# Kernel optimization log

Measured on AMD Instinct MI355X. Metric: run time of the kernel, lower is better.

## Reference

```python
import jax, jax.numpy as jnp
import numpy as np

# Dimensions (must match init_kwargs)
IC = 8    # independent channels (one Linear each)
RC = 8    # regular channels
PC = 8    # parallel channels
G = 4     # shared-weight groups
IPG = 512 // G   # input length per group = 128
OPG = 512 // G   # output length per group = 128
B = 128


def setup_inputs() -> dict:
    key = jax.random.key(0)
    k1, k2, k3 = jax.random.split(key, 3)
    x = jax.random.normal(k1, (B, IC * RC, PC, IPG * G), dtype=jnp.float32)
    # Per-independent-channel Linear weights/biases (torch Linear: y = x @ W.T + b)
    bound = 1.0 / np.sqrt(IPG)
    W = jax.random.uniform(k2, (IC, OPG, IPG), dtype=jnp.float32, minval=-bound, maxval=bound)
    b = jax.random.uniform(k3, (IC, OPG), dtype=jnp.float32, minval=-bound, maxval=bound)
    return {"x": x, "W": W, "b": b}


def reference(x, W, b):
    Bx = x.shape[0]
    # view -> (B, IC, RC, PC, IPG*G); tensor_split along last + stack(dim=-2)
    # is a contiguous reshape -> (B, IC, RC, PC, G, IPG)
    xi = x.reshape(Bx, IC, RC, PC, G, IPG)
    # block-diagonal grouped GEMM: one Linear per independent channel i
    y = jnp.einsum('bicpgk,iok->bicpgo', xi, W) + b[None, :, None, None, None, :]
    # (B, IC, RC, PC, G, OPG) -> (B, IC*RC, PC, G*OPG)
    return y.reshape(Bx, IC * RC, PC, G * OPG)
```

## Files before the change

kernel.cpp:

```cpp
#include <hip/hip_runtime.h>
#include <hip/hip_bf16.h>

typedef __bf16 bf16x8 __attribute__((ext_vector_type(8)));
typedef __bf16 bf16x4 __attribute__((ext_vector_type(4)));
typedef float floatx4 __attribute__((ext_vector_type(4)));

#define IC 8
#define RC 8
#define PC 8
#define G_ 4
#define IPG 128
#define OPG 128

#define WROW 136
#define XROW 136

__global__ __launch_bounds__(256, 3)
void mcsl_kernel(const float* __restrict__ x,
                 const float* __restrict__ W,
                 const float* __restrict__ bias,
                 float* __restrict__ y)
{
    __shared__ __align__(16) __bf16 Wlds[128 * WROW];
    __shared__ __align__(16) __bf16 Xlds[64 * XROW];
    __shared__ float blds[128];

    const int tid = threadIdx.x;
    const int i = blockIdx.x & 7;
    const int b = blockIdx.x >> 3;

    const float* xbase = x + ((size_t)(b * (IC * RC) + i * RC)) * (PC * G_ * IPG);
    float*       ybase = y + ((size_t)(b * (IC * RC) + i * RC)) * (PC * G_ * OPG);

    const float4* Wsrc = (const float4*)(W + (size_t)i * (OPG * IPG));
    #pragma unroll
    for (int it = 0; it < 16; ++it) {
        int idx = tid + it * 256;
        float4 w4 = Wsrc[idx];
        int o  = idx >> 5;
        int k4 = (idx & 31) << 2;
        bf16x4 wq;
        wq[0] = (__bf16)w4.x; wq[1] = (__bf16)w4.y;
        wq[2] = (__bf16)w4.z; wq[3] = (__bf16)w4.w;
        *(bf16x4*)&Wlds[o * WROW + k4] = wq;
    }
    if (tid < 128) blds[tid] = bias[i * OPG + tid];

    float4 pf[8];
    {
        const float4* src = (const float4*)xbase;
        #pragma unroll
        for (int j = 0; j < 8; ++j) pf[j] = src[tid * 8 + j];
    }
    {
        const int row = tid >> 2, col0 = (tid & 3) * 32;
        #pragma unroll
        for (int j = 0; j < 4; ++j) {
            float4 a0 = pf[2 * j], a1 = pf[2 * j + 1];
            bf16x8 v;
            v[0] = (__bf16)a0.x; v[1] = (__bf16)a0.y; v[2] = (__bf16)a0.z; v[3] = (__bf16)a0.w;
            v[4] = (__bf16)a1.x; v[5] = (__bf16)a1.y; v[6] = (__bf16)a1.z; v[7] = (__bf16)a1.w;
            *(bf16x8*)&Xlds[row * XROW + col0 + j * 8] = v;
        }
    }
    __syncthreads();

    const int lane = tid & 63;
    const int wv   = tid >> 6;
    const int nrow = lane & 15;
    const int quad = lane >> 4;

    #pragma unroll
    for (int c = 0; c < 4; ++c) {
        if (c < 3) {
            const float4* src = (const float4*)(xbase + (size_t)(c + 1) * 64 * IPG);
            #pragma unroll
            for (int j = 0; j < 8; ++j) pf[j] = src[tid * 8 + j];
        }

        bf16x8 af[4];
        #pragma unroll
        for (int ks = 0; ks < 4; ++ks)
            af[ks] = *(const bf16x8*)&Xlds[(wv * 16 + nrow) * XROW + ks * 32 + quad * 8];

        floatx4 acc[8];
        #pragma unroll
        for (int ct = 0; ct < 8; ++ct) acc[ct] = (floatx4){0.f, 0.f, 0.f, 0.f};

        #pragma unroll
        for (int ks = 0; ks < 4; ++ks) {
            #pragma unroll
            for (int ct = 0; ct < 8; ++ct) {
                bf16x8 bfrag = *(const bf16x8*)&Wlds[(ct * 16 + nrow) * WROW + ks * 32 + quad * 8];
                acc[ct] = __builtin_amdgcn_mfma_f32_16x16x32_bf16(af[ks], bfrag, acc[ct], 0, 0, 0);
            }
        }

        if (c < 3) {
            __syncthreads();
            const int row = tid >> 2, col0 = (tid & 3) * 32;
            #pragma unroll
            for (int j = 0; j < 4; ++j) {
                float4 a0 = pf[2 * j], a1 = pf[2 * j + 1];
                bf16x8 v;
                v[0] = (__bf16)a0.x; v[1] = (__bf16)a0.y; v[2] = (__bf16)a0.z; v[3] = (__bf16)a0.w;
                v[4] = (__bf16)a1.x; v[5] = (__bf16)a1.y; v[6] = (__bf16)a1.z; v[7] = (__bf16)a1.w;
                *(bf16x8*)&Xlds[row * XROW + col0 + j * 8] = v;
            }
            __syncthreads();
        }

        float* yc = ybase + (size_t)c * 64 * OPG;
        const int rowl = wv * 16 + quad * 4;
        #pragma unroll
        for (int ct = 0; ct < 8; ++ct) {
            float bo = blds[ct * 16 + nrow];
            #pragma unroll
            for (int r = 0; r < 4; ++r)
                yc[(size_t)(rowl + r) * OPG + ct * 16 + nrow] = acc[ct][r] + bo;
        }
    }
}

extern "C" void kernel_launch(void* const* d_in, const int* in_sizes, int n_in,
                              void* d_out, int out_size, void* d_ws, size_t ws_size,
                              hipStream_t stream) {
    const float* x = (const float*)d_in[0];
    const float* W = (const float*)d_in[1];
    const float* b = (const float*)d_in[2];
    float* y = (float*)d_out;
    dim3 grid(1024), block(256);
    hipLaunchKernelGGL(mcsl_kernel, grid, block, 0, stream, x, W, b, y);
}
```

Measured before the change: 247.0 us.

## Hold W fragments in registers and stream X directly from global per wave

Each block now covers two batches. Every wave loads its W fragments from LDS into registers once, then streams 16-row X tiles straight from global memory into MFMA B operands. It double-buffers those loads with register prefetch, which drops the X staging through LDS and its block-wide barriers. Bias is folded into the accumulator init and the output goes out as vector nontemporal stores after swapping MFMA operand roles. In exchange the kernel uses many more registers (launch bounds cut to 2 blocks), half as many blocks, and uncoalesced-ish 32-byte global reads.

```diff
diff --git a/kernel.cpp b/kernel.cpp
--- a/kernel.cpp
+++ b/kernel.cpp
@@ -13,24 +13,19 @@
 #define OPG 128
 
 #define WROW 136
-#define XROW 136
 
-__global__ __launch_bounds__(256, 3)
+__global__ __launch_bounds__(256, 2)
 void mcsl_kernel(const float* __restrict__ x,
                  const float* __restrict__ W,
                  const float* __restrict__ bias,
                  float* __restrict__ y)
 {
     __shared__ __align__(16) __bf16 Wlds[128 * WROW];
-    __shared__ __align__(16) __bf16 Xlds[64 * XROW];
-    __shared__ float blds[128];
+    __shared__ __align__(16) float blds[128];
 
     const int tid = threadIdx.x;
     const int i = blockIdx.x & 7;
-    const int b = blockIdx.x >> 3;
-
-    const float* xbase = x + ((size_t)(b * (IC * RC) + i * RC)) * (PC * G_ * IPG);
-    float*       ybase = y + ((size_t)(b * (IC * RC) + i * RC)) * (PC * G_ * OPG);
+    const int j = blockIdx.x >> 3;
 
     const float4* Wsrc = (const float4*)(W + (size_t)i * (OPG * IPG));
     #pragma unroll
@@ -45,24 +40,6 @@
         *(bf16x4*)&Wlds[o * WROW + k4] = wq;
     }
     if (tid < 128) blds[tid] = bias[i * OPG + tid];
-
-    float4 pf[8];
-    {
-        const float4* src = (const float4*)xbase;
-        #pragma unroll
-        for (int j = 0; j < 8; ++j) pf[j] = src[tid * 8 + j];
-    }
-    {
-        const int row = tid >> 2, col0 = (tid & 3) * 32;
-        #pragma unroll
-        for (int j = 0; j < 4; ++j) {
-            float4 a0 = pf[2 * j], a1 = pf[2 * j + 1];
-            bf16x8 v;
-            v[0] = (__bf16)a0.x; v[1] = (__bf16)a0.y; v[2] = (__bf16)a0.z; v[3] = (__bf16)a0.w;
-            v[4] = (__bf16)a1.x; v[5] = (__bf16)a1.y; v[6] = (__bf16)a1.z; v[7] = (__bf16)a1.w;
-            *(bf16x8*)&Xlds[row * XROW + col0 + j * 8] = v;
-        }
-    }
     __syncthreads();
 
     const int lane = tid & 63;
@@ -70,56 +47,78 @@
     const int nrow = lane & 15;
     const int quad = lane >> 4;
 
+    bf16x8 wfrag[8][4];
     #pragma unroll
-    for (int c = 0; c < 4; ++c) {
-        if (c < 3) {
-            const float4* src = (const float4*)(xbase + (size_t)(c + 1) * 64 * IPG);
-            #pragma unroll
-            for (int j = 0; j < 8; ++j) pf[j] = src[tid * 8 + j];
-        }
-
-        bf16x8 af[4];
+    for (int ct = 0; ct < 8; ++ct)
         #pragma unroll
         for (int ks = 0; ks < 4; ++ks)
-            af[ks] = *(const bf16x8*)&Xlds[(wv * 16 + nrow) * XROW + ks * 32 + quad * 8];
+            wfrag[ct][ks] = *(const bf16x8*)&Wlds[(ct * 16 + nrow) * WROW + ks * 32 + quad * 8];
 
-        floatx4 acc[8];
-        #pragma unroll
-        for (int ct = 0; ct < 8; ++ct) acc[ct] = (floatx4){0.f, 0.f, 0.f, 0.f};
+    const int b = 2 * j + (wv >> 1);
+    const size_t slab = ((size_t)(b * (IC * RC) + i * RC)) * (PC * G_ * IPG);
+    const int rhalf = (wv & 1) * 128;
 
+    const float4* xs = (const float4*)(x + slab);
+    float*        ys = y + slab;
+
+#define TILE_SRC(T) (xs + (size_t)(rhalf + (T) * 16 + nrow) * 32 + quad * 2)
+
+    float4 pfA[8], pfB[8];
+    {
+        const float4* s0 = TILE_SRC(0);
+        const float4* s1 = TILE_SRC(1);
         #pragma unroll
         for (int ks = 0; ks < 4; ++ks) {
-            #pragma unroll
-            for (int ct = 0; ct < 8; ++ct) {
-                bf16x8 bfrag = *(const bf16x8*)&Wlds[(ct * 16 + nrow) * WROW + ks * 32 + quad * 8];
-                acc[ct] = __builtin_amdgcn_mfma_f32_16x16x32_bf16(af[ks], bfrag, acc[ct], 0, 0, 0);
-            }
+            pfA[2 * ks]     = s0[ks * 8];
+            pfA[2 * ks + 1] = s0[ks * 8 + 1];
         }
-
-        if (c < 3) {
-            __syncthreads();
-            const int row = tid >> 2, col0 = (tid & 3) * 32;
-            #pragma unroll
-            for (int j = 0; j < 4; ++j) {
-                float4 a0 = pf[2 * j], a1 = pf[2 * j + 1];
-                bf16x8 v;
-                v[0] = (__bf16)a0.x; v[1] = (__bf16)a0.y; v[2] = (__bf16)a0.z; v[3] = (__bf16)a0.w;
-                v[4] = (__bf16)a1.x; v[5] = (__bf16)a1.y; v[6] = (__bf16)a1.z; v[7] = (__bf16)a1.w;
-                *(bf16x8*)&Xlds[row * XROW + col0 + j * 8] = v;
-            }
-            __syncthreads();
-        }
-
-        float* yc = ybase + (size_t)c * 64 * OPG;
-        const int rowl = wv * 16 + quad * 4;
         #pragma unroll
-        for (int ct = 0; ct < 8; ++ct) {
-            float bo = blds[ct * 16 + nrow];
-            #pragma unroll
-            for (int r = 0; r < 4; ++r)
-                yc[(size_t)(rowl + r) * OPG + ct * 16 + nrow] = acc[ct][r] + bo;
+        for (int ks = 0; ks < 4; ++ks) {
+            pfB[2 * ks]     = s1[ks * 8];
+            pfB[2 * ks + 1] = s1[ks * 8 + 1];
         }
     }
+
+#define TILE_STEP(T, BUF, PREF) do {                                            \
+        floatx4 acc[8];                                                         \
+        _Pragma("unroll")                                                       \
+        for (int ct = 0; ct < 8; ++ct)                                          \
+            acc[ct] = *(const floatx4*)&blds[ct * 16 + quad * 4];               \
+        const float4* nsrc = (PREF) ? TILE_SRC((T) + 2) : xs;                   \
+        _Pragma("unroll")                                                       \
+        for (int ks = 0; ks < 4; ++ks) {                                        \
+            float4 a0 = BUF[2 * ks], a1 = BUF[2 * ks + 1];                      \
+            if (PREF) {                                                         \
+                BUF[2 * ks]     = nsrc[ks * 8];                                 \
+                BUF[2 * ks + 1] = nsrc[ks * 8 + 1];                             \
+            }                                                                   \
+            bf16x8 v;                                                           \
+            v[0] = (__bf16)a0.x; v[1] = (__bf16)a0.y;                           \
+            v[2] = (__bf16)a0.z; v[3] = (__bf16)a0.w;                           \
+            v[4] = (__bf16)a1.x; v[5] = (__bf16)a1.y;                           \
+            v[6] = (__bf16)a1.z; v[7] = (__bf16)a1.w;                           \
+            _Pragma("unroll")                                                   \
+            for (int ct = 0; ct < 8; ++ct)                                      \
+                acc[ct] = __builtin_amdgcn_mfma_f32_16x16x32_bf16(              \
+                              wfrag[ct][ks], v, acc[ct], 0, 0, 0);              \
+        }                                                                       \
+        float* yrow = ys + (size_t)(rhalf + (T) * 16 + nrow) * OPG + quad * 4;  \
+        _Pragma("unroll")                                                       \
+        for (int ct = 0; ct < 8; ++ct)                                          \
+            __builtin_nontemporal_store(acc[ct], (floatx4*)(yrow + ct * 16));   \
+    } while (0)
+
+    TILE_STEP(0, pfA, 1);
+    TILE_STEP(1, pfB, 1);
+    TILE_STEP(2, pfA, 1);
+    TILE_STEP(3, pfB, 1);
+    TILE_STEP(4, pfA, 1);
+    TILE_STEP(5, pfB, 1);
+    TILE_STEP(6, pfA, 0);
+    TILE_STEP(7, pfB, 0);
+
+#undef TILE_STEP
+#undef TILE_SRC
 }
 
 extern "C" void kernel_launch(void* const* d_in, const int* in_sizes, int n_in,
@@ -129,6 +128,6 @@
     const float* W = (const float*)d_in[1];
     const float* b = (const float*)d_in[2];
     float* y = (float*)d_out;
-    dim3 grid(1024), block(256);
+    dim3 grid(512), block(256);
     hipLaunchKernelGGL(mcsl_kernel, grid, block, 0, stream, x, W, b, y);
 }
```

New measurement: 249.2 us. No clear change (+0.9%).

## Load X fragments directly to registers and swap MFMA operands for vector stores

Applied to the files above, without the earlier changes.

Drops the X staging buffer in LDS. Each wave now loads its input rows straight into registers in MFMA fragment layout and converts them to bf16 there. The MFMA operands are swapped (W as A, X as B) so each lane holds four consecutive output columns, which allows 16-byte vectorized stores in place of scalar strided ones. Bias is preloaded into the accumulators, and the block-to-row mapping is changed. Less LDS per block permits a higher occupancy hint, at the risk of less coalesced global reads of x, since each lane reads 32-byte chunks spread over rows.

```diff
diff --git a/kernel.cpp b/kernel.cpp
--- a/kernel.cpp
+++ b/kernel.cpp
@@ -5,120 +5,107 @@
 typedef __bf16 bf16x4 __attribute__((ext_vector_type(4)));
 typedef float floatx4 __attribute__((ext_vector_type(4)));
 
-#define IC 8
-#define RC 8
-#define PC 8
-#define G_ 4
-#define IPG 128
-#define OPG 128
+#define WPITCH 272
 
-#define WROW 136
-#define XROW 136
-
-__global__ __launch_bounds__(256, 3)
+__global__ __launch_bounds__(256, 4)
 void mcsl_kernel(const float* __restrict__ x,
                  const float* __restrict__ W,
                  const float* __restrict__ bias,
                  float* __restrict__ y)
 {
-    __shared__ __align__(16) __bf16 Wlds[128 * WROW];
-    __shared__ __align__(16) __bf16 Xlds[64 * XROW];
-    __shared__ float blds[128];
+    __shared__ __align__(16) unsigned char Wl[128 * WPITCH];
+    __shared__ __align__(16) float blds[128];
 
-    const int tid = threadIdx.x;
-    const int i = blockIdx.x & 7;
-    const int b = blockIdx.x >> 3;
-
-    const float* xbase = x + ((size_t)(b * (IC * RC) + i * RC)) * (PC * G_ * IPG);
-    float*       ybase = y + ((size_t)(b * (IC * RC) + i * RC)) * (PC * G_ * OPG);
-
-    const float4* Wsrc = (const float4*)(W + (size_t)i * (OPG * IPG));
-    #pragma unroll
-    for (int it = 0; it < 16; ++it) {
-        int idx = tid + it * 256;
-        float4 w4 = Wsrc[idx];
-        int o  = idx >> 5;
-        int k4 = (idx & 31) << 2;
-        bf16x4 wq;
-        wq[0] = (__bf16)w4.x; wq[1] = (__bf16)w4.y;
-        wq[2] = (__bf16)w4.z; wq[3] = (__bf16)w4.w;
-        *(bf16x4*)&Wlds[o * WROW + k4] = wq;
-    }
-    if (tid < 128) blds[tid] = bias[i * OPG + tid];
-
-    float4 pf[8];
-    {
-        const float4* src = (const float4*)xbase;
-        #pragma unroll
-        for (int j = 0; j < 8; ++j) pf[j] = src[tid * 8 + j];
-    }
-    {
-        const int row = tid >> 2, col0 = (tid & 3) * 32;
-        #pragma unroll
-        for (int j = 0; j < 4; ++j) {
-            float4 a0 = pf[2 * j], a1 = pf[2 * j + 1];
-            bf16x8 v;
-            v[0] = (__bf16)a0.x; v[1] = (__bf16)a0.y; v[2] = (__bf16)a0.z; v[3] = (__bf16)a0.w;
-            v[4] = (__bf16)a1.x; v[5] = (__bf16)a1.y; v[6] = (__bf16)a1.z; v[7] = (__bf16)a1.w;
-            *(bf16x8*)&Xlds[row * XROW + col0 + j * 8] = v;
-        }
-    }
-    __syncthreads();
-
+    const int tid  = threadIdx.x;
+    const int i    = blockIdx.x & 7;
+    const int j    = blockIdx.x >> 3;
     const int lane = tid & 63;
     const int wv   = tid >> 6;
     const int nrow = lane & 15;
     const int quad = lane >> 4;
 
+    {
+        const float4* Wsrc = (const float4*)(W + (size_t)i * 16384);
+        #pragma unroll
+        for (int it = 0; it < 16; ++it) {
+            int idx = tid + it * 256;
+            float4 w4 = Wsrc[idx];
+            int o  = idx >> 5;
+            int kb = (idx & 31) * 8;
+            bf16x4 wq;
+            wq[0] = (__bf16)w4.x; wq[1] = (__bf16)w4.y;
+            wq[2] = (__bf16)w4.z; wq[3] = (__bf16)w4.w;
+            *(bf16x4*)&Wl[o * WPITCH + kb] = wq;
+        }
+        if (tid < 128) blds[tid] = bias[i * 128 + tid];
+    }
+    __syncthreads();
+
+    const int jh = j >> 4;
+    const int s  = j & 15;
+
+    float4 pf[8];
+    {
+        const int b0 = wv * 8 + jh;
+        const float4* sp = (const float4*)(x + ((size_t)(b0 * 8 + i) * 32768
+                                                + s * 2048))
+                         + nrow * 32 + quad * 2;
+        #pragma unroll
+        for (int ks = 0; ks < 4; ++ks) {
+            pf[2 * ks]     = sp[ks * 8];
+            pf[2 * ks + 1] = sp[ks * 8 + 1];
+        }
+    }
+
     #pragma unroll
-    for (int c = 0; c < 4; ++c) {
-        if (c < 3) {
-            const float4* src = (const float4*)(xbase + (size_t)(c + 1) * 64 * IPG);
-            #pragma unroll
-            for (int j = 0; j < 8; ++j) pf[j] = src[tid * 8 + j];
+    for (int r = 0; r < 4; ++r) {
+        const int b = (4 * r + wv) * 8 + jh;
+
+        bf16x8 xf[4];
+        #pragma unroll
+        for (int ks = 0; ks < 4; ++ks) {
+            float4 a0 = pf[2 * ks], a1 = pf[2 * ks + 1];
+            bf16x8 v;
+            v[0] = (__bf16)a0.x; v[1] = (__bf16)a0.y;
+            v[2] = (__bf16)a0.z; v[3] = (__bf16)a0.w;
+            v[4] = (__bf16)a1.x; v[5] = (__bf16)a1.y;
+            v[6] = (__bf16)a1.z; v[7] = (__bf16)a1.w;
+            xf[ks] = v;
         }
 
-        bf16x8 af[4];
-        #pragma unroll
-        for (int ks = 0; ks < 4; ++ks)
-            af[ks] = *(const bf16x8*)&Xlds[(wv * 16 + nrow) * XROW + ks * 32 + quad * 8];
+        if (r < 3) {
+            const int bn = (4 * (r + 1) + wv) * 8 + jh;
+            const float4* sp = (const float4*)(x + ((size_t)(bn * 8 + i) * 32768
+                                                    + s * 2048))
+                             + nrow * 32 + quad * 2;
+            #pragma unroll
+            for (int ks = 0; ks < 4; ++ks) {
+                pf[2 * ks]     = sp[ks * 8];
+                pf[2 * ks + 1] = sp[ks * 8 + 1];
+            }
+        }
 
         floatx4 acc[8];
         #pragma unroll
-        for (int ct = 0; ct < 8; ++ct) acc[ct] = (floatx4){0.f, 0.f, 0.f, 0.f};
+        for (int ct = 0; ct < 8; ++ct)
+            acc[ct] = *(const floatx4*)&blds[ct * 16 + quad * 4];
 
         #pragma unroll
         for (int ks = 0; ks < 4; ++ks) {
             #pragma unroll
             for (int ct = 0; ct < 8; ++ct) {
-                bf16x8 bfrag = *(const bf16x8*)&Wlds[(ct * 16 + nrow) * WROW + ks * 32 + quad * 8];
-                acc[ct] = __builtin_amdgcn_mfma_f32_16x16x32_bf16(af[ks], bfrag, acc[ct], 0, 0, 0);
+                bf16x8 wf = *(const bf16x8*)&Wl[(ct * 16 + nrow) * WPITCH
+                                                + ks * 64 + quad * 16];
+                acc[ct] = __builtin_amdgcn_mfma_f32_16x16x32_bf16(
+                              wf, xf[ks], acc[ct], 0, 0, 0);
             }
         }
 
-        if (c < 3) {
-            __syncthreads();
-            const int row = tid >> 2, col0 = (tid & 3) * 32;
-            #pragma unroll
-            for (int j = 0; j < 4; ++j) {
-                float4 a0 = pf[2 * j], a1 = pf[2 * j + 1];
-                bf16x8 v;
-                v[0] = (__bf16)a0.x; v[1] = (__bf16)a0.y; v[2] = (__bf16)a0.z; v[3] = (__bf16)a0.w;
-                v[4] = (__bf16)a1.x; v[5] = (__bf16)a1.y; v[6] = (__bf16)a1.z; v[7] = (__bf16)a1.w;
-                *(bf16x8*)&Xlds[row * XROW + col0 + j * 8] = v;
-            }
-            __syncthreads();
-        }
-
-        float* yc = ybase + (size_t)c * 64 * OPG;
-        const int rowl = wv * 16 + quad * 4;
+        float* yr = y + ((size_t)(b * 8 + i) * 32768 + s * 2048)
+                  + nrow * 128 + quad * 4;
         #pragma unroll
-        for (int ct = 0; ct < 8; ++ct) {
-            float bo = blds[ct * 16 + nrow];
-            #pragma unroll
-            for (int r = 0; r < 4; ++r)
-                yc[(size_t)(rowl + r) * OPG + ct * 16 + nrow] = acc[ct][r] + bo;
-        }
+        for (int ct = 0; ct < 8; ++ct)
+            *(floatx4*)(yr + ct * 16) = acc[ct];
     }
 }
 
```

Measured after the change: 245.7 us. No clear change (-0.5%).
